# Kernel optimization log

Measured on AMD Instinct MI355X. Metric: run time of the kernel, lower is better.

The kernel has to match this reference:

```python
import jax, jax.numpy as jnp
import numpy as np

SMOOTH = 9.0
EPS = 1e-8
LEAK = 0.1  # LeakyReLU slope used by SCAN_attention


def setup_inputs() -> dict:
    key = jax.random.key(0)
    k1, k2, k3, k4 = jax.random.split(key, 4)
    n_img, n_reg, d = 256, 36, 1024
    n_cap, max_w = 256, 60
    imgs = jax.random.normal(k1, (n_img, n_reg, d), dtype=jnp.float32)
    caps = jax.random.normal(k2, (n_cap, max_w, d), dtype=jnp.float32)
    img_lens = jax.random.randint(k3, (n_img,), 1, n_reg + 1, dtype=jnp.int32)
    cap_lens = jax.random.randint(k4, (n_cap,), 5, max_w + 1, dtype=jnp.int32)
    return {"imgs": imgs, "caps": caps, "img_lens": img_lens, "cap_lens": cap_lens}


def reference(imgs, caps, img_lens, cap_lens):
    # imgs: (I, R, D); caps: (C, W, D); cap_lens: (C,)
    C, W, D = caps.shape
    mask = (jnp.arange(W)[None, :] < cap_lens[:, None]).astype(caps.dtype)  # (C, W)
    # Zero padded words: equivalent to the per-caption slicing in the torch loop
    q = caps * mask[:, :, None]

    # SCAN attention, vectorized over captions and images.
    # raw scores: context . query^T  -> (C, I, W, R)
    s = jnp.einsum('cwd,ird->ciwr', q, imgs)
    s = jnp.where(s >= 0, s, LEAK * s)  # LeakyReLU(0.1)
    # l2norm over the word dim (padded words contribute exactly 0)
    norm = jnp.sqrt(jnp.sum(s * s, axis=2, keepdims=True)) + EPS
    s = s / norm
    attn = jax.nn.softmax(s * SMOOTH, axis=3)  # softmax over regions
    wctx = jnp.einsum('ciwr,ird->ciwd', attn, imgs)  # (C, I, W, D)

    # cosine similarity over feature dim
    w12 = jnp.einsum('cwd,ciwd->ciw', q, wctx)
    w1 = jnp.sqrt(jnp.sum(q * q, axis=-1))[:, None, :]          # (C, 1, W)
    w2 = jnp.sqrt(jnp.sum(wctx * wctx, axis=-1))                # (C, I, W)
    sim = w12 / jnp.maximum(w1 * w2, EPS)                       # (C, I, W)

    # masked mean over valid words (matches per-caption mean over n_word)
    col = jnp.sum(sim * mask[:, None, :], axis=2) / cap_lens.astype(sim.dtype)[:, None]
    return col.T  # (n_image, n_caption)
```

## Files before the change

### kernel.cpp

```cpp
#include <hip/hip_runtime.h>


#define NIMG 256
#define NREG 36
#define DIM 1024
#define NCAP 256
#define MAXW 60
#define WPAD 64

typedef short bf16x8 __attribute__((ext_vector_type(8)));
typedef float f32x4 __attribute__((ext_vector_type(4)));

__device__ __forceinline__ unsigned short f2bf(float f) {
  unsigned u = __float_as_uint(f);
  u += 0x7FFF + ((u >> 16) & 1);
  return (unsigned short)(u >> 16);
}

__global__ void k_sort(const int* __restrict__ cap_lens, int* __restrict__ perm,
                       float* __restrict__ w1sq) {
  const int i = threadIdx.x;
#pragma unroll
  for (int j = 0; j < WPAD; ++j) w1sq[i * WPAD + j] = 0.f;
  const int li = cap_lens[i];
  int r = 0;
  for (int j = 0; j < NCAP; ++j) {
    const int lj = cap_lens[j];
    r += (lj < li) || (lj == li && j < i);
  }
  perm[r] = i;
}

__global__ void k_prep_caps_frag(const float* __restrict__ caps, const int* __restrict__ cap_lens,
                                 unsigned short* __restrict__ qbfF,
                                 float* __restrict__ w1sq) {
  const int k32 = blockIdx.x;
  const int c = blockIdx.y;
  const int t = threadIdx.x;
  const int mt = t >> 6;
  const int lane = t & 63;
  const int m = mt * 16 + (lane & 15);
  const int k0 = k32 * 32 + (lane >> 4) * 8;
  const int clen = cap_lens[c];
  float4 v0 = make_float4(0.f, 0.f, 0.f, 0.f), v1 = v0;
  if (m < clen && m < MAXW) {
    const float* src = caps + ((size_t)c * MAXW + m) * DIM + k0;
    v0 = *reinterpret_cast<const float4*>(src);
    v1 = *reinterpret_cast<const float4*>(src + 4);
  }
  float ss = v0.x * v0.x + v0.y * v0.y + v0.z * v0.z + v0.w * v0.w
           + v1.x * v1.x + v1.y * v1.y + v1.z * v1.z + v1.w * v1.w;
  ss += __shfl_xor(ss, 16);
  ss += __shfl_xor(ss, 32);
  if ((lane >> 4) == 0 && ss != 0.f) atomicAdd(&w1sq[(size_t)c * WPAD + m], ss);
  ushort4 o0, o1;
  o0.x = f2bf(v0.x); o0.y = f2bf(v0.y); o0.z = f2bf(v0.z); o0.w = f2bf(v0.w);
  o1.x = f2bf(v1.x); o1.y = f2bf(v1.y); o1.z = f2bf(v1.z); o1.w = f2bf(v1.w);
  unsigned short* dst = qbfF + ((size_t)(((c * 32 + k32) * 4 + mt) * 64 + lane)) * 8;
  *reinterpret_cast<ushort4*>(dst) = o0;
  *reinterpret_cast<ushort4*>(dst + 4) = o1;
}

__global__ void k_prep_imgs_frag(const float* __restrict__ imgs,
                                 unsigned short* __restrict__ ibfF) {
  const int k32 = blockIdx.x;
  const int i = blockIdx.y;
  const int t = threadIdx.x;
  const int nt = t >> 6;
  const int lane = t & 63;
  const int r = nt * 16 + (lane & 15);
  const int k0 = k32 * 32 + (lane >> 4) * 8;
  float4 v0 = make_float4(0.f, 0.f, 0.f, 0.f), v1 = v0;
  if (r < NREG) {
    const float* src = imgs + ((size_t)i * NREG + r) * DIM + k0;
    v0 = *reinterpret_cast<const float4*>(src);
    v1 = *reinterpret_cast<const float4*>(src + 4);
  }
  ushort4 o0, o1;
  o0.x = f2bf(v0.x); o0.y = f2bf(v0.y); o0.z = f2bf(v0.z); o0.w = f2bf(v0.w);
  o1.x = f2bf(v1.x); o1.y = f2bf(v1.y); o1.z = f2bf(v1.z); o1.w = f2bf(v1.w);
  unsigned short* dst = ibfF + ((size_t)(((i * 32 + k32) * 3 + nt) * 64 + lane)) * 8;
  *reinterpret_cast<ushort4*>(dst) = o0;
  *reinterpret_cast<ushort4*>(dst + 4) = o1;
}

__global__ void k_gram_mfma(const float* __restrict__ imgs,
                            const unsigned short* __restrict__ ibfF,
                            unsigned short* __restrict__ gbf,
                            float* __restrict__ gdiag) {
  const int i = blockIdx.x;
  const int lane = threadIdx.x & 63;
  const int l15 = lane & 15;
  const int quad = lane >> 4;

  float* dg = gdiag + (size_t)i * 48;
#pragma unroll
  for (int r0 = 0; r0 < 36; r0 += 4) {
    const int r = r0 + quad;
    const float* row = imgs + ((size_t)i * NREG + r) * DIM;
    float ss = 0.f;
#pragma unroll
    for (int p = 0; p < 16; ++p) {
      float4 v = *reinterpret_cast<const float4*>(row + p * 64 + l15 * 4);
      ss += v.x * v.x + v.y * v.y + v.z * v.z + v.w * v.w;
    }
    ss += __shfl_xor(ss, 1); ss += __shfl_xor(ss, 2);
    ss += __shfl_xor(ss, 4); ss += __shfl_xor(ss, 8);
    if (l15 == 0) dg[r] = ss;
  }
  if (lane < 12) dg[36 + lane] = 0.f;

  const unsigned short* base = ibfF + ((size_t)i * 32 * 3) * 512 + lane * 8;
  const f32x4 zero4 = {0.f, 0.f, 0.f, 0.f};
  f32x4 acc[3][3];
#pragma unroll
  for (int na = 0; na < 3; ++na)
#pragma unroll
    for (int nb = 0; nb < 3; ++nb) acc[na][nb] = zero4;
  bf16x8 f[2][3];
#pragma unroll
  for (int nt = 0; nt < 3; ++nt)
    f[0][nt] = *reinterpret_cast<const bf16x8*>(base + (size_t)nt * 512);
#pragma unroll
  for (int k32 = 0; k32 < 32; ++k32) {
    if (k32 + 1 < 32) {
      const int nb_ = (k32 + 1) & 1;
#pragma unroll
      for (int nt = 0; nt < 3; ++nt)
        f[nb_][nt] = *reinterpret_cast<const bf16x8*>(base + ((size_t)(k32 + 1) * 3 + nt) * 512);
    }
    const int b = k32 & 1;
#pragma unroll
    for (int na = 0; na < 3; ++na)
#pragma unroll
      for (int nb = 0; nb < 3; ++nb)
        acc[na][nb] = __builtin_amdgcn_mfma_f32_16x16x32_bf16(f[b][na], f[b][nb], acc[na][nb], 0, 0, 0);
  }
  unsigned short* g = gbf + (size_t)i * (48 * 64);
#pragma unroll
  for (int na = 0; na < 3; ++na)
#pragma unroll
    for (int nb = 0; nb < 3; ++nb)
#pragma unroll
      for (int rg = 0; rg < 4; ++rg) {
        const int r = na * 16 + quad * 4 + rg;
        const int c = nb * 16 + l15;
        g[r * 64 + c] = (r == c) ? (unsigned short)0 : f2bf(acc[na][nb][rg]);
      }
  for (int idx = lane; idx < 96; idx += 64) {
    const int r = idx >> 1, half = idx & 1;
    *reinterpret_cast<uint4*>(g + r * 64 + 48 + half * 8) = make_uint4(0, 0, 0, 0);
  }
}

template <int MLIM>
__device__ __forceinline__ void kloopT(const unsigned short* __restrict__ aBase,
                                       const unsigned short* __restrict__ bBase,
                                       const int lane8,
                                       f32x4 (&acc)[3][4]) {
  bf16x8 fa[3][MLIM], fb[3][3];
  auto load = [&](int k32, int buf) __attribute__((always_inline)) {
#pragma unroll
    for (int nt = 0; nt < 3; ++nt)
      fb[buf][nt] = *reinterpret_cast<const bf16x8*>(bBase + (size_t)k32 * 1536 + nt * 512 + lane8);
#pragma unroll
    for (int mt = 0; mt < MLIM; ++mt)
      fa[buf][mt] = *reinterpret_cast<const bf16x8*>(aBase + (size_t)k32 * 2048 + mt * 512 + lane8);
  };
  auto compute = [&](int buf) __attribute__((always_inline)) {
#pragma unroll
    for (int mt = 0; mt < MLIM; ++mt)
#pragma unroll
      for (int nt = 0; nt < 3; ++nt)
        acc[nt][mt] = __builtin_amdgcn_mfma_f32_16x16x32_bf16(fb[buf][nt], fa[buf][mt], acc[nt][mt], 0, 0, 0);
  };
  load(0, 0);
  load(1, 1);
#pragma unroll
  for (int k32 = 0; k32 < 32; ++k32) {
    if (k32 + 2 < 32) load(k32 + 2, (k32 + 2) % 3);
    __builtin_amdgcn_sched_barrier(0);
    compute(k32 % 3);
  }
}

__launch_bounds__(256, 3)
__global__ void k_main(const unsigned short* __restrict__ qbfF,
                       const unsigned short* __restrict__ ibfF,
                       const float* __restrict__ w1sq,
                       const unsigned short* __restrict__ gbf,
                       const float* __restrict__ gdiag,
                       const int* __restrict__ cap_lens,
                       const int* __restrict__ perm,
                       float* __restrict__ out) {
  __shared__ struct {
    unsigned short attn[4][4096];
    float w12[4][64];
    float w2d[4][64];
    float w2x[4][64];
  } lds;
  const int tid = threadIdx.x;
  const int lane = tid & 63;
  const int wv = tid >> 6;
  const int l15 = lane & 15;
  const int quad = lane >> 4;
  const int flat = blockIdx.y * (NIMG / 2) + blockIdx.x;
  const int xcd = flat & 7;
  const int idx = flat >> 3;
  const int bx = xcd * 16 + (idx & 15);
  const int by = idx >> 4;
  const int i0 = bx * 2;
  const int cA = perm[2 * by], cB = perm[2 * by + 1];
  const int c = __builtin_amdgcn_readfirstlane((wv & 1) ? cB : cA);
  const int img = __builtin_amdgcn_readfirstlane(i0 + (wv >> 1));
  const int clen = cap_lens[c];
  const int mlim = __builtin_amdgcn_readfirstlane((clen + 15) >> 4);

  f32x4 acc[3][4];
  const f32x4 zero4 = {0.f, 0.f, 0.f, 0.f};
#pragma unroll
  for (int nt = 0; nt < 3; ++nt)
#pragma unroll
    for (int mt = 0; mt < 4; ++mt) acc[nt][mt] = zero4;

  const unsigned short* aBase = qbfF + (size_t)c * (32 * 4 * 512);
  const unsigned short* bBase = ibfF + (size_t)img * (32 * 3 * 512);
  const int lane8 = lane * 8;

  switch (mlim) {
    case 1: kloopT<1>(aBase, bBase, lane8, acc); break;
    case 2: kloopT<2>(aBase, bBase, lane8, acc); break;
    case 3: kloopT<3>(aBase, bBase, lane8, acc); break;
    default: kloopT<4>(aBase, bBase, lane8, acc); break;
  }

  {
    uint4* ab = reinterpret_cast<uint4*>(&lds.attn[wv][0]);
    const uint4 z4 = make_uint4(0, 0, 0, 0);
    for (int j = lane; j < 512; j += 64) ab[j] = z4;
  }

  const float* dg = gdiag + (size_t)img * 48;
  float dv[3][4];
#pragma unroll
  for (int nt = 0; nt < 3; ++nt)
#pragma unroll
    for (int rg = 0; rg < 4; ++rg)
      dv[nt][rg] = dg[nt * 16 + quad * 4 + rg];

  float scale[3][4];
#pragma unroll
  for (int nt = 0; nt < 3; ++nt)
#pragma unroll
    for (int rg = 0; rg < 4; ++rg) {
      float p = 0.f;
#pragma unroll
      for (int mt = 0; mt < 4; ++mt)
        if (mt < mlim) {
          const float s = acc[nt][mt][rg];
          const float l = s < 0.f ? 0.1f * s : s;
          p += l * l;
        }
      p += __shfl_xor(p, 1); p += __shfl_xor(p, 2);
      p += __shfl_xor(p, 4); p += __shfl_xor(p, 8);
      scale[nt][rg] = 9.0f / (sqrtf(p) + 1e-8f);
    }

  unsigned a_pk[4][3][2];
#pragma unroll
  for (int mt = 0; mt < 4; ++mt) {
    if (mt >= mlim) continue;
    float ee[3][4];
    float sm = 0.f, wp = 0.f, dd = 0.f;
#pragma unroll
    for (int nt = 0; nt < 3; ++nt) {
      const bool rvalid = (nt < 2) || (quad == 0);
#pragma unroll
      for (int rg = 0; rg < 4; ++rg) {
        const float s = acc[nt][mt][rg];
        const float l = s < 0.f ? 0.1f * s : s;
        const float e0 = rvalid ? __expf(l * scale[nt][rg]) : 0.f;
        ee[nt][rg] = e0;
        sm += e0;
        wp += e0 * s;
        dd += e0 * e0 * dv[nt][rg];
      }
    }
    sm += __shfl_xor(sm, 16); sm += __shfl_xor(sm, 32);
    wp += __shfl_xor(wp, 16); wp += __shfl_xor(wp, 32);
    dd += __shfl_xor(dd, 16); dd += __shfl_xor(dd, 32);
    const float inv = 1.0f / sm;
    const int w = mt * 16 + l15;
    const int key = l15 & 7;
    unsigned short* arow = &lds.attn[wv][w * 64];
#pragma unroll
    for (int nt = 0; nt < 3; ++nt)
#pragma unroll
      for (int pr = 0; pr < 2; ++pr) {
        const unsigned b0 = f2bf(ee[nt][2 * pr] * inv);
        const unsigned b1 = f2bf(ee[nt][2 * pr + 1] * inv);
        const unsigned pk = b0 | (b1 << 16);
        a_pk[mt][nt][pr] = pk;
        const int r0 = nt * 16 + quad * 4 + 2 * pr;
        *reinterpret_cast<unsigned*>(&arow[(((r0 >> 3) ^ key) << 3) + (r0 & 7)]) = pk;
      }
    if (quad == 0) { lds.w12[wv][w] = wp * inv; lds.w2d[wv][w] = dd * inv * inv; }
  }

  const unsigned short* gBase = gbf + (size_t)img * (48 * 64);
  bf16x8 gfrag[3][2];
#pragma unroll
  for (int nt = 0; nt < 3; ++nt)
#pragma unroll
    for (int ks = 0; ks < 2; ++ks)
      gfrag[nt][ks] = *reinterpret_cast<const bf16x8*>(
          gBase + (nt * 16 + l15) * 64 + ((ks * 4 + quad) << 3));
#pragma unroll
  for (int mt = 0; mt < 4; ++mt) {
    if (mt >= mlim) continue;
    bf16x8 af[2];
#pragma unroll
    for (int ks = 0; ks < 2; ++ks)
      af[ks] = *reinterpret_cast<const bf16x8*>(
          &lds.attn[wv][(mt * 16 + l15) * 64 + (((ks * 4 + quad) ^ (l15 & 7)) << 3)]);
    f32x4 Yt[3] = {zero4, zero4, zero4};
#pragma unroll
    for (int nt = 0; nt < 3; ++nt)
#pragma unroll
      for (int ks = 0; ks < 2; ++ks)
        Yt[nt] = __builtin_amdgcn_mfma_f32_16x16x32_bf16(gfrag[nt][ks], af[ks], Yt[nt], 0, 0, 0);
    float p = 0.f;
#pragma unroll
    for (int nt = 0; nt < 3; ++nt)
#pragma unroll
      for (int pr = 0; pr < 2; ++pr) {
        const unsigned pk = a_pk[mt][nt][pr];
        const float a0 = __uint_as_float(pk << 16);
        const float a1 = __uint_as_float(pk & 0xffff0000u);
        p += a0 * Yt[nt][2 * pr] + a1 * Yt[nt][2 * pr + 1];
      }
    p += __shfl_xor(p, 16); p += __shfl_xor(p, 32);
    if (quad == 0) lds.w2x[wv][mt * 16 + l15] = p;
  }

  const float* w1Base = w1sq + (size_t)c * WPAD;
  float simv = 0.f;
  if (lane < clen) {
    const float w2sq = fmaxf(lds.w2x[wv][lane] + lds.w2d[wv][lane], 0.f);
    const float w2v = sqrtf(w2sq);
    const float w12v = lds.w12[wv][lane];
    const float w1v = sqrtf(w1Base[lane]);
    simv = w12v / fmaxf(w1v * w2v, 1e-8f);
  }
  simv += __shfl_xor(simv, 1);
  simv += __shfl_xor(simv, 2);
  simv += __shfl_xor(simv, 4);
  simv += __shfl_xor(simv, 8);
  simv += __shfl_xor(simv, 16);
  simv += __shfl_xor(simv, 32);
  if (lane == 0) out[(size_t)img * NCAP + c] = simv / (float)clen;
}

extern "C" void kernel_launch(void* const* d_in, const int* in_sizes, int n_in,
                              void* d_out, int out_size, void* d_ws, size_t ws_size,
                              hipStream_t stream) {
  const float* imgs = (const float*)d_in[0];
  const float* caps = (const float*)d_in[1];
  const int* cap_lens = (const int*)d_in[3];
  float* out = (float*)d_out;

  char* ws = (char*)d_ws;
  const size_t QBF_B = (size_t)NCAP * 32 * 4 * 512 * 2;
  const size_t IBF_B = (size_t)NIMG * 32 * 3 * 512 * 2;
  const size_t W1_B = (size_t)NCAP * WPAD * 4;
  const size_t GBF_B = (size_t)NIMG * 48 * 64 * 2;
  const size_t GD_B = (size_t)NIMG * 48 * 4;
  unsigned short* qbfF = (unsigned short*)ws;
  unsigned short* ibfF = (unsigned short*)(ws + QBF_B);
  float* w1sq = (float*)(ws + QBF_B + IBF_B);
  unsigned short* gbf = (unsigned short*)(ws + QBF_B + IBF_B + W1_B);
  float* gdiag = (float*)(ws + QBF_B + IBF_B + W1_B + GBF_B);
  int* perm = (int*)(ws + QBF_B + IBF_B + W1_B + GBF_B + GD_B);

  k_sort<<<1, NCAP, 0, stream>>>(cap_lens, perm, w1sq);
  k_prep_caps_frag<<<dim3(32, NCAP), 256, 0, stream>>>(caps, cap_lens, qbfF, w1sq);
  k_prep_imgs_frag<<<dim3(32, NIMG), 192, 0, stream>>>(imgs, ibfF);
  k_gram_mfma<<<NIMG, 64, 0, stream>>>(imgs, ibfF, gbf, gdiag);
  k_main<<<dim3(NIMG / 2, NCAP / 2), 256, 0, stream>>>(qbfF, ibfF, w1sq, gbf, gdiag, cap_lens, perm, out);
}
```

Baseline: 530.3 us.

## Process two images per wave to reuse caption fragments in the score GEMM

Each wave now computes scores for two images against one caption, so every caption fragment it loads feeds twice as many MFMAs. The grid is halved along the image axis and the epilogue loops over the two images. The accumulators double, so the k-loop prefetch drops from triple to double buffering and launch bounds go from 3 to 2 blocks per CU. The cost is lower occupancy and less latency hiding on the fragment loads.

After: 513.1 us. 1.03x faster.

```diff
diff --git a/kernel.cpp b/kernel.cpp
--- a/kernel.cpp
+++ b/kernel.cpp
@@ -154,37 +154,42 @@
 }
 
 template <int MLIM>
-__device__ __forceinline__ void kloopT(const unsigned short* __restrict__ aBase,
-                                       const unsigned short* __restrict__ bBase,
-                                       const int lane8,
-                                       f32x4 (&acc)[3][4]) {
-  bf16x8 fa[3][MLIM], fb[3][3];
+__device__ __forceinline__ void kloopT2(const unsigned short* __restrict__ aBase,
+                                        const unsigned short* __restrict__ bBase,
+                                        const int lane8,
+                                        f32x4 (&acc)[2][3][4]) {
+  bf16x8 fa[2][MLIM], fb[2][2][3];
   auto load = [&](int k32, int buf) __attribute__((always_inline)) {
 #pragma unroll
-    for (int nt = 0; nt < 3; ++nt)
-      fb[buf][nt] = *reinterpret_cast<const bf16x8*>(bBase + (size_t)k32 * 1536 + nt * 512 + lane8);
+    for (int im = 0; im < 2; ++im)
+#pragma unroll
+      for (int nt = 0; nt < 3; ++nt)
+        fb[buf][im][nt] = *reinterpret_cast<const bf16x8*>(
+            bBase + (size_t)im * (32 * 3 * 512) + (size_t)k32 * 1536 + nt * 512 + lane8);
 #pragma unroll
     for (int mt = 0; mt < MLIM; ++mt)
       fa[buf][mt] = *reinterpret_cast<const bf16x8*>(aBase + (size_t)k32 * 2048 + mt * 512 + lane8);
   };
   auto compute = [&](int buf) __attribute__((always_inline)) {
 #pragma unroll
-    for (int mt = 0; mt < MLIM; ++mt)
-#pragma unroll
-      for (int nt = 0; nt < 3; ++nt)
-        acc[nt][mt] = __builtin_amdgcn_mfma_f32_16x16x32_bf16(fb[buf][nt], fa[buf][mt], acc[nt][mt], 0, 0, 0);
+    for (int im = 0; im < 2; ++im)
+#pragma unroll
+      for (int mt = 0; mt < MLIM; ++mt)
+#pragma unroll
+        for (int nt = 0; nt < 3; ++nt)
+          acc[im][nt][mt] = __builtin_amdgcn_mfma_f32_16x16x32_bf16(
+              fb[buf][im][nt], fa[buf][mt], acc[im][nt][mt], 0, 0, 0);
   };
   load(0, 0);
-  load(1, 1);
 #pragma unroll
   for (int k32 = 0; k32 < 32; ++k32) {
-    if (k32 + 2 < 32) load(k32 + 2, (k32 + 2) % 3);
+    if (k32 + 1 < 32) load(k32 + 1, (k32 + 1) & 1);
     __builtin_amdgcn_sched_barrier(0);
-    compute(k32 % 3);
-  }
-}
-
-__launch_bounds__(256, 3)
+    compute(k32 & 1);
+  }
+}
+
+__launch_bounds__(256, 2)
 __global__ void k_main(const unsigned short* __restrict__ qbfF,
                        const unsigned short* __restrict__ ibfF,
                        const float* __restrict__ w1sq,
@@ -204,34 +209,36 @@
   const int wv = tid >> 6;
   const int l15 = lane & 15;
   const int quad = lane >> 4;
-  const int flat = blockIdx.y * (NIMG / 2) + blockIdx.x;
+  const int flat = blockIdx.y * (NIMG / 4) + blockIdx.x;
   const int xcd = flat & 7;
   const int idx = flat >> 3;
-  const int bx = xcd * 16 + (idx & 15);
-  const int by = idx >> 4;
-  const int i0 = bx * 2;
+  const int bx = xcd * 8 + (idx & 7);
+  const int by = idx >> 3;
+  const int i0 = bx * 4;
   const int cA = perm[2 * by], cB = perm[2 * by + 1];
   const int c = __builtin_amdgcn_readfirstlane((wv & 1) ? cB : cA);
-  const int img = __builtin_amdgcn_readfirstlane(i0 + (wv >> 1));
+  const int imgBase = __builtin_amdgcn_readfirstlane(i0 + (wv >> 1) * 2);
   const int clen = cap_lens[c];
   const int mlim = __builtin_amdgcn_readfirstlane((clen + 15) >> 4);
 
-  f32x4 acc[3][4];
+  f32x4 acc[2][3][4];
   const f32x4 zero4 = {0.f, 0.f, 0.f, 0.f};
 #pragma unroll
-  for (int nt = 0; nt < 3; ++nt)
-#pragma unroll
-    for (int mt = 0; mt < 4; ++mt) acc[nt][mt] = zero4;
+  for (int im = 0; im < 2; ++im)
+#pragma unroll
+    for (int nt = 0; nt < 3; ++nt)
+#pragma unroll
+      for (int mt = 0; mt < 4; ++mt) acc[im][nt][mt] = zero4;
 
   const unsigned short* aBase = qbfF + (size_t)c * (32 * 4 * 512);
-  const unsigned short* bBase = ibfF + (size_t)img * (32 * 3 * 512);
+  const unsigned short* bBase = ibfF + (size_t)imgBase * (32 * 3 * 512);
   const int lane8 = lane * 8;
 
   switch (mlim) {
-    case 1: kloopT<1>(aBase, bBase, lane8, acc); break;
-    case 2: kloopT<2>(aBase, bBase, lane8, acc); break;
-    case 3: kloopT<3>(aBase, bBase, lane8, acc); break;
-    default: kloopT<4>(aBase, bBase, lane8, acc); break;
+    case 1: kloopT2<1>(aBase, bBase, lane8, acc); break;
+    case 2: kloopT2<2>(aBase, bBase, lane8, acc); break;
+    case 3: kloopT2<3>(aBase, bBase, lane8, acc); break;
+    default: kloopT2<4>(aBase, bBase, lane8, acc); break;
   }
 
   {
@@ -239,126 +246,130 @@
     const uint4 z4 = make_uint4(0, 0, 0, 0);
     for (int j = lane; j < 512; j += 64) ab[j] = z4;
   }
-
-  const float* dg = gdiag + (size_t)img * 48;
-  float dv[3][4];
-#pragma unroll
-  for (int nt = 0; nt < 3; ++nt)
-#pragma unroll
-    for (int rg = 0; rg < 4; ++rg)
-      dv[nt][rg] = dg[nt * 16 + quad * 4 + rg];
-
-  float scale[3][4];
-#pragma unroll
-  for (int nt = 0; nt < 3; ++nt)
-#pragma unroll
-    for (int rg = 0; rg < 4; ++rg) {
+  const float* w1Base = w1sq + (size_t)c * WPAD;
+
+#pragma unroll
+  for (int im = 0; im < 2; ++im) {
+    const int img = imgBase + im;
+    const float* dg = gdiag + (size_t)img * 48;
+    float dv[3][4];
+#pragma unroll
+    for (int nt = 0; nt < 3; ++nt)
+#pragma unroll
+      for (int rg = 0; rg < 4; ++rg)
+        dv[nt][rg] = dg[nt * 16 + quad * 4 + rg];
+
+    float scale[3][4];
+#pragma unroll
+    for (int nt = 0; nt < 3; ++nt)
+#pragma unroll
+      for (int rg = 0; rg < 4; ++rg) {
+        float p = 0.f;
+#pragma unroll
+        for (int mt = 0; mt < 4; ++mt)
+          if (mt < mlim) {
+            const float s = acc[im][nt][mt][rg];
+            const float l = s < 0.f ? 0.1f * s : s;
+            p += l * l;
+          }
+        p += __shfl_xor(p, 1); p += __shfl_xor(p, 2);
+        p += __shfl_xor(p, 4); p += __shfl_xor(p, 8);
+        scale[nt][rg] = 9.0f / (sqrtf(p) + 1e-8f);
+      }
+
+    unsigned a_pk[4][3][2];
+#pragma unroll
+    for (int mt = 0; mt < 4; ++mt) {
+      if (mt >= mlim) continue;
+      float ee[3][4];
+      float sm = 0.f, wp = 0.f, dd = 0.f;
+#pragma unroll
+      for (int nt = 0; nt < 3; ++nt) {
+        const bool rvalid = (nt < 2) || (quad == 0);
+#pragma unroll
+        for (int rg = 0; rg < 4; ++rg) {
+          const float s = acc[im][nt][mt][rg];
+          const float l = s < 0.f ? 0.1f * s : s;
+          const float e0 = rvalid ? __expf(l * scale[nt][rg]) : 0.f;
+          ee[nt][rg] = e0;
+          sm += e0;
+          wp += e0 * s;
+          dd += e0 * e0 * dv[nt][rg];
+        }
+      }
+      sm += __shfl_xor(sm, 16); sm += __shfl_xor(sm, 32);
+      wp += __shfl_xor(wp, 16); wp += __shfl_xor(wp, 32);
+      dd += __shfl_xor(dd, 16); dd += __shfl_xor(dd, 32);
+      const float inv = 1.0f / sm;
+      const int w = mt * 16 + l15;
+      const int key = l15 & 7;
+      unsigned short* arow = &lds.attn[wv][w * 64];
+#pragma unroll
+      for (int nt = 0; nt < 3; ++nt)
+#pragma unroll
+        for (int pr = 0; pr < 2; ++pr) {
+          const unsigned b0 = f2bf(ee[nt][2 * pr] * inv);
+          const unsigned b1 = f2bf(ee[nt][2 * pr + 1] * inv);
+          const unsigned pk = b0 | (b1 << 16);
+          a_pk[mt][nt][pr] = pk;
+          const int r0 = nt * 16 + quad * 4 + 2 * pr;
+          *reinterpret_cast<unsigned*>(&arow[(((r0 >> 3) ^ key) << 3) + (r0 & 7)]) = pk;
+        }
+      if (quad == 0) { lds.w12[wv][w] = wp * inv; lds.w2d[wv][w] = dd * inv * inv; }
+    }
+
+    const unsigned short* gBase = gbf + (size_t)img * (48 * 64);
+    bf16x8 gfrag[3][2];
+#pragma unroll
+    for (int nt = 0; nt < 3; ++nt)
+#pragma unroll
+      for (int ks = 0; ks < 2; ++ks)
+        gfrag[nt][ks] = *reinterpret_cast<const bf16x8*>(
+            gBase + (nt * 16 + l15) * 64 + ((ks * 4 + quad) << 3));
+#pragma unroll
+    for (int mt = 0; mt < 4; ++mt) {
+      if (mt >= mlim) continue;
+      bf16x8 af[2];
+#pragma unroll
+      for (int ks = 0; ks < 2; ++ks)
+        af[ks] = *reinterpret_cast<const bf16x8*>(
+            &lds.attn[wv][(mt * 16 + l15) * 64 + (((ks * 4 + quad) ^ (l15 & 7)) << 3)]);
+      f32x4 Yt[3] = {zero4, zero4, zero4};
+#pragma unroll
+      for (int nt = 0; nt < 3; ++nt)
+#pragma unroll
+        for (int ks = 0; ks < 2; ++ks)
+          Yt[nt] = __builtin_amdgcn_mfma_f32_16x16x32_bf16(gfrag[nt][ks], af[ks], Yt[nt], 0, 0, 0);
       float p = 0.f;
 #pragma unroll
-      for (int mt = 0; mt < 4; ++mt)
-        if (mt < mlim) {
-          const float s = acc[nt][mt][rg];
-          const float l = s < 0.f ? 0.1f * s : s;
-          p += l * l;
+      for (int nt = 0; nt < 3; ++nt)
+#pragma unroll
+        for (int pr = 0; pr < 2; ++pr) {
+          const unsigned pk = a_pk[mt][nt][pr];
+          const float a0 = __uint_as_float(pk << 16);
+          const float a1 = __uint_as_float(pk & 0xffff0000u);
+          p += a0 * Yt[nt][2 * pr] + a1 * Yt[nt][2 * pr + 1];
         }
-      p += __shfl_xor(p, 1); p += __shfl_xor(p, 2);
-      p += __shfl_xor(p, 4); p += __shfl_xor(p, 8);
-      scale[nt][rg] = 9.0f / (sqrtf(p) + 1e-8f);
+      p += __shfl_xor(p, 16); p += __shfl_xor(p, 32);
+      if (quad == 0) lds.w2x[wv][mt * 16 + l15] = p;
     }
 
-  unsigned a_pk[4][3][2];
-#pragma unroll
-  for (int mt = 0; mt < 4; ++mt) {
-    if (mt >= mlim) continue;
-    float ee[3][4];
-    float sm = 0.f, wp = 0.f, dd = 0.f;
-#pragma unroll
-    for (int nt = 0; nt < 3; ++nt) {
-      const bool rvalid = (nt < 2) || (quad == 0);
-#pragma unroll
-      for (int rg = 0; rg < 4; ++rg) {
-        const float s = acc[nt][mt][rg];
-        const float l = s < 0.f ? 0.1f * s : s;
-        const float e0 = rvalid ? __expf(l * scale[nt][rg]) : 0.f;
-        ee[nt][rg] = e0;
-        sm += e0;
-        wp += e0 * s;
-        dd += e0 * e0 * dv[nt][rg];
-      }
+    float simv = 0.f;
+    if (lane < clen) {
+      const float w2sq = fmaxf(lds.w2x[wv][lane] + lds.w2d[wv][lane], 0.f);
+      const float w2v = sqrtf(w2sq);
+      const float w12v = lds.w12[wv][lane];
+      const float w1v = sqrtf(w1Base[lane]);
+      simv = w12v / fmaxf(w1v * w2v, 1e-8f);
     }
-    sm += __shfl_xor(sm, 16); sm += __shfl_xor(sm, 32);
-    wp += __shfl_xor(wp, 16); wp += __shfl_xor(wp, 32);
-    dd += __shfl_xor(dd, 16); dd += __shfl_xor(dd, 32);
-    const float inv = 1.0f / sm;
-    const int w = mt * 16 + l15;
-    const int key = l15 & 7;
-    unsigned short* arow = &lds.attn[wv][w * 64];
-#pragma unroll
-    for (int nt = 0; nt < 3; ++nt)
-#pragma unroll
-      for (int pr = 0; pr < 2; ++pr) {
-        const unsigned b0 = f2bf(ee[nt][2 * pr] * inv);
-        const unsigned b1 = f2bf(ee[nt][2 * pr + 1] * inv);
-        const unsigned pk = b0 | (b1 << 16);
-        a_pk[mt][nt][pr] = pk;
-        const int r0 = nt * 16 + quad * 4 + 2 * pr;
-        *reinterpret_cast<unsigned*>(&arow[(((r0 >> 3) ^ key) << 3) + (r0 & 7)]) = pk;
-      }
-    if (quad == 0) { lds.w12[wv][w] = wp * inv; lds.w2d[wv][w] = dd * inv * inv; }
-  }
-
-  const unsigned short* gBase = gbf + (size_t)img * (48 * 64);
-  bf16x8 gfrag[3][2];
-#pragma unroll
-  for (int nt = 0; nt < 3; ++nt)
-#pragma unroll
-    for (int ks = 0; ks < 2; ++ks)
-      gfrag[nt][ks] = *reinterpret_cast<const bf16x8*>(
-          gBase + (nt * 16 + l15) * 64 + ((ks * 4 + quad) << 3));
-#pragma unroll
-  for (int mt = 0; mt < 4; ++mt) {
-    if (mt >= mlim) continue;
-    bf16x8 af[2];
-#pragma unroll
-    for (int ks = 0; ks < 2; ++ks)
-      af[ks] = *reinterpret_cast<const bf16x8*>(
-          &lds.attn[wv][(mt * 16 + l15) * 64 + (((ks * 4 + quad) ^ (l15 & 7)) << 3)]);
-    f32x4 Yt[3] = {zero4, zero4, zero4};
-#pragma unroll
-    for (int nt = 0; nt < 3; ++nt)
-#pragma unroll
-      for (int ks = 0; ks < 2; ++ks)
-        Yt[nt] = __builtin_amdgcn_mfma_f32_16x16x32_bf16(gfrag[nt][ks], af[ks], Yt[nt], 0, 0, 0);
-    float p = 0.f;
-#pragma unroll
-    for (int nt = 0; nt < 3; ++nt)
-#pragma unroll
-      for (int pr = 0; pr < 2; ++pr) {
-        const unsigned pk = a_pk[mt][nt][pr];
-        const float a0 = __uint_as_float(pk << 16);
-        const float a1 = __uint_as_float(pk & 0xffff0000u);
-        p += a0 * Yt[nt][2 * pr] + a1 * Yt[nt][2 * pr + 1];
-      }
-    p += __shfl_xor(p, 16); p += __shfl_xor(p, 32);
-    if (quad == 0) lds.w2x[wv][mt * 16 + l15] = p;
-  }
-
-  const float* w1Base = w1sq + (size_t)c * WPAD;
-  float simv = 0.f;
-  if (lane < clen) {
-    const float w2sq = fmaxf(lds.w2x[wv][lane] + lds.w2d[wv][lane], 0.f);
-    const float w2v = sqrtf(w2sq);
-    const float w12v = lds.w12[wv][lane];
-    const float w1v = sqrtf(w1Base[lane]);
-    simv = w12v / fmaxf(w1v * w2v, 1e-8f);
-  }
-  simv += __shfl_xor(simv, 1);
-  simv += __shfl_xor(simv, 2);
-  simv += __shfl_xor(simv, 4);
-  simv += __shfl_xor(simv, 8);
-  simv += __shfl_xor(simv, 16);
-  simv += __shfl_xor(simv, 32);
-  if (lane == 0) out[(size_t)img * NCAP + c] = simv / (float)clen;
+    simv += __shfl_xor(simv, 1);
+    simv += __shfl_xor(simv, 2);
+    simv += __shfl_xor(simv, 4);
+    simv += __shfl_xor(simv, 8);
+    simv += __shfl_xor(simv, 16);
+    simv += __shfl_xor(simv, 32);
+    if (lane == 0) out[(size_t)img * NCAP + c] = simv / (float)clen;
+  }
 }
 
 extern "C" void kernel_launch(void* const* d_in, const int* in_sizes, int n_in,
@@ -386,5 +397,5 @@
   k_prep_caps_frag<<<dim3(32, NCAP), 256, 0, stream>>>(caps, cap_lens, qbfF, w1sq);
   k_prep_imgs_frag<<<dim3(32, NIMG), 192, 0, stream>>>(imgs, ibfF);
   k_gram_mfma<<<NIMG, 64, 0, stream>>>(imgs, ibfF, gbf, gdiag);
-  k_main<<<dim3(NIMG / 2, NCAP / 2), 256, 0, stream>>>(qbfF, ibfF, w1sq, gbf, gdiag, cap_lens, perm, out);
-}
+  k_main<<<dim3(NIMG / 4, NCAP / 2), 256, 0, stream>>>(qbfF, ibfF, w1sq, gbf, gdiag, cap_lens, perm, out);
+}
```
